# Kernel optimization log

Measured on AMD Instinct MI355X. Metric: run time of the kernel, lower is better.

The kernel has to match this reference:

```python
import jax, jax.numpy as jnp
import numpy as np

B = 256          # batch of molecules
N_ATOM = 1024    # atoms per molecule
N_EDGE = 8192    # directed edges per molecule (avg degree 8)
NEG_SLOPE = 0.01 # torch LeakyReLU default


def setup_inputs() -> dict:
    key = jax.random.key(0)
    ks = jax.random.split(key, 8)
    x = jax.random.normal(ks[0], (B, 3 * N_ATOM), dtype=jnp.float32)
    edge_index = jax.random.randint(ks[1], (2, N_EDGE), 0, N_ATOM, dtype=jnp.int64)
    # GCNConv weights (Glorot-ish small scale) and biases
    W1 = jax.random.normal(ks[2], (3, 64), dtype=jnp.float32) * 0.3
    b1 = jnp.zeros((64,), jnp.float32)
    W2 = jax.random.normal(ks[3], (64, 64), dtype=jnp.float32) * 0.1
    b2 = jnp.zeros((64,), jnp.float32)
    # project MLP: Linear(64,128) + LeakyReLU
    Wp = jax.random.normal(ks[4], (64, 128), dtype=jnp.float32) * 0.1
    bp = jnp.zeros((128,), jnp.float32)
    return {"x": x, "edge_index": edge_index, "W1": W1, "b1": b1,
            "W2": W2, "b2": b2, "Wp": Wp, "bp": bp}


def _leaky_relu(v):
    return jnp.where(v >= 0, v, NEG_SLOPE * v)


def reference(x, edge_index, W1, b1, W2, b2, Wp, bp):
    # x: [B, 3*n_atom] -> node features [B, n_atom, 3]
    bsz, n_feat = x.shape
    n = n_feat // 3
    h = x.reshape(bsz, n, 3)

    src = edge_index[0]  # message sources
    dst = edge_index[1]  # aggregation targets

    # GCN normalization with self-loops: deg[i] = 1 + in-degree(i)
    ones_e = jnp.ones((src.shape[0],), x.dtype)
    deg = jax.ops.segment_sum(ones_e, dst, num_segments=n) + 1.0
    dinv = jax.lax.rsqrt(deg)                # deg^{-1/2}, deg >= 1
    norm_e = dinv[src] * dinv[dst]           # [E]
    norm_self = dinv * dinv                  # self-loop weight per node

    def gcn(h, W, b):
        hw = h @ W                                        # [B, n, d_out]
        msg = hw[:, src, :] * norm_e[None, :, None]       # [B, E, d_out]
        agg = jax.vmap(lambda m: jax.ops.segment_sum(m, dst, num_segments=n))(msg)
        return agg + norm_self[None, :, None] * hw + b

    h = _leaky_relu(gcn(h, W1, b1))
    h = _leaky_relu(gcn(h, W2, b2))

    # global_mean_pool: every graph has exactly n atoms -> mean over atom axis
    g = h.mean(axis=1)                                    # [B, 64]

    # project MLP: Linear + LeakyReLU
    return _leaky_relu(g @ Wp + bp)                       # [B, 128]
```

## Files before the change

### kernel.cpp

```cpp
#include <hip/hip_runtime.h>

#define N_ATOMS 1024
#define N_EDGES 8192
#define EPAD    (N_EDGES + N_ATOMS)
#define NBATCH  256
#define NEG     0.01f

typedef unsigned int u32;
typedef __attribute__((ext_vector_type(2))) float f32x2;
typedef __attribute__((ext_vector_type(4))) float f32x4;
typedef __attribute__((ext_vector_type(8))) _Float16 f16x8;

__device__ __forceinline__ u32 pkrtz(float lo, float hi) {
    u32 r;
    asm("v_cvt_pkrtz_f16_f32 %0, %1, %2" : "=v"(r) : "v"(lo), "v"(hi));
    return r;
}
#define FMIX_LO(a, w, u) \
    asm("v_fma_mix_f32 %0, %1, %2, %0 op_sel_hi:[0,1,0]" : "+v"(a) : "v"(w), "v"(u))
#define FMIX_HI(a, w, u) \
    asm("v_fma_mix_f32 %0, %1, %2, %0 op_sel:[0,1,0] op_sel_hi:[0,1,0]" : "+v"(a) : "v"(w), "v"(u))

#define META_OFF   0
#define COLW_OFF   8192
#define SELFW_OFF  (8192 + 73728)
#define IPERM_OFF  (SELFW_OFF + 4096)
#define W2T_OFF    (IPERM_OFF + 4096)

#define TSTR_B 144
#define SM_TILE_BYTES (N_ATOMS * TSTR_B)
#define SM_CT_OFF SM_TILE_BYTES
#define SM_TOTAL (SM_TILE_BYTES + 16384)

__global__ __launch_bounds__(1024) void build_csr(
    const int* __restrict__ ei,
    int2* __restrict__ colw,
    int2* __restrict__ meta,
    float* __restrict__ selfw_s,
    int*  __restrict__ iperm_g,
    u32*  __restrict__ w2t,
    const float* __restrict__ W2)
{
    __shared__ int   sdeg[N_ATOMS];
    __shared__ int   sstart[N_ATOMS];
    __shared__ int   siperm[N_ATOMS];
    __shared__ float sdinv[N_ATOMS];
    __shared__ int   wtot[16];
    __shared__ int   hist[128];
    const int t = threadIdx.x;
    const int lane = t & 63;
    const int w = t >> 6;
    const int* srcA = ei;
    const int* dstA = ei + N_EDGES;

    sdeg[t] = 0;
    if (t < 128) hist[t] = 0;
    __syncthreads();
    for (int e = t; e < N_EDGES; e += 1024) atomicAdd(&sdeg[dstA[e]], 1);
    __syncthreads();

    const int deg  = sdeg[t];
    const int pdeg = (deg + 1) & ~1;
    int v = pdeg;
    #pragma unroll
    for (int d = 1; d < 64; d <<= 1) {
        int u = __shfl_up(v, d, 64);
        if (lane >= d) v += u;
    }
    if (lane == 63) wtot[w] = v;
    __syncthreads();
    if (t == 0) {
        int run = 0;
        #pragma unroll
        for (int i = 0; i < 16; ++i) { int c = wtot[i]; wtot[i] = run; run += c; }
    }
    __syncthreads();
    const int start = v - pdeg + wtot[w];
    sstart[t] = start;
    const float dv = rsqrtf((float)deg + 1.0f);
    sdinv[t] = dv;
    if (deg & 1) colw[start + deg] = make_int2(0, 0);

    #pragma unroll
    for (int i = 0; i < 2; ++i) {
        const int idx = t + i * 1024;
        const int c = idx >> 5, kk = idx & 31;
        w2t[c * 32 + kk] = pkrtz(W2[(2 * kk) * 64 + c], W2[(2 * kk + 1) * 64 + c]);
    }

    const int dcl = deg < 127 ? deg : 127;
    atomicAdd(&hist[dcl], 1);
    __syncthreads();
    if (t == 0) {
        int run = 0;
        for (int i = 0; i < 128; ++i) { int c = hist[i]; hist[i] = run; run += c; }
    }
    __syncthreads();
    const int pos = atomicAdd(&hist[dcl], 1);
    siperm[t] = pos;
    iperm_g[t] = pos;
    meta[pos] = make_int2(start, pdeg >> 1);
    selfw_s[pos] = dv * dv;
    sdeg[t] = 0;
    __syncthreads();

    for (int e = t; e < N_EDGES; e += 1024) {
        const int d = dstA[e];
        const int s = srcA[e];
        const int slot = atomicAdd(&sdeg[d], 1);
        const float wgt = sdinv[s] * sdinv[d];
        colw[sstart[d] + slot] = make_int2(siperm[s], __float_as_int(wgt));
    }
}

__global__ __launch_bounds__(1024, 4) void gnn_main(
    const float* __restrict__ x,
    const int2* __restrict__ meta,
    const int2* __restrict__ colw,
    const float* __restrict__ selfw_s,
    const int*  __restrict__ iperm_g,
    const float* __restrict__ W1, const float* __restrict__ b1,
    const u32*  __restrict__ w2t, const float* __restrict__ b2,
    const float* __restrict__ Wp, const float* __restrict__ bp,
    float* __restrict__ out)
{
    extern __shared__ char smem[];
    float4* ctile4 = (float4*)(smem + SM_CT_OFF);
    float*  paux   = (float*)ctile4;
    float*  wpool  = paux;
    float*  gvec   = paux + 1024;
    float*  proj   = paux + 1088;

    const int t = threadIdx.x;
    const int b = blockIdx.x;
    const float* xb = x + (size_t)b * (3 * N_ATOMS);

    {
        const int ip = iperm_g[t];
        float4 c;
        c.x = xb[3 * t]; c.y = xb[3 * t + 1]; c.z = xb[3 * t + 2]; c.w = 0.0f;
        ctile4[ip] = c;
    }
    __syncthreads();

    {
        const int2 mt = meta[t];
        const int s0 = mt.x, np1 = mt.y;
        const float sw = selfw_s[t];
        const float4 cs = ctile4[t];
        float A0 = sw * cs.x, A1 = sw * cs.y, A2 = sw * cs.z;
        int4 cur = make_int4(0, 0, 0, 0);
        if (np1 > 0) cur = *(const int4*)(colw + s0);
        for (int jj = 0; jj < np1; ++jj) {
            const int4 nxt = (jj + 1 < np1) ? *(const int4*)(colw + s0 + 2 * (jj + 1)) : cur;
            const float4 c0 = ctile4[cur.x];
            const float4 c1 = ctile4[cur.z];
            const float w0 = __int_as_float(cur.y), w1 = __int_as_float(cur.w);
            A0 += w0 * c0.x + w1 * c1.x;
            A1 += w0 * c0.y + w1 * c1.y;
            A2 += w0 * c0.z + w1 * c1.z;
            cur = nxt;
        }
        u32 pw[32];
        #pragma unroll
        for (int p = 0; p < 32; ++p) {
            f32x2 vv = *(const f32x2*)(b1 + 2 * p);
            vv = __builtin_elementwise_fma((f32x2){A0, A0}, *(const f32x2*)(W1 + 2 * p), vv);
            vv = __builtin_elementwise_fma((f32x2){A1, A1}, *(const f32x2*)(W1 + 64 + 2 * p), vv);
            vv = __builtin_elementwise_fma((f32x2){A2, A2}, *(const f32x2*)(W1 + 128 + 2 * p), vv);
            vv.x = fmaxf(vv.x, NEG * vv.x);
            vv.y = fmaxf(vv.y, NEG * vv.y);
            pw[p] = pkrtz(vv.x, vv.y);
        }
        uint4* trow = (uint4*)(smem + (size_t)t * TSTR_B);
        #pragma unroll
        for (int q = 0; q < 8; ++q)
            trow[q] = make_uint4(pw[4 * q], pw[4 * q + 1], pw[4 * q + 2], pw[4 * q + 3]);
    }

    const int w   = t >> 6;
    const int g   = (t & 63) >> 3;
    const int m   = t & 7;
    const int mo  = m * 16;

    int s0a[8], npa[8];
    float swa[8];
    #pragma unroll
    for (int k = 0; k < 8; ++k) {
        const int slot = k * 128 + w * 8 + g;
        const int2 mk = meta[slot];
        s0a[k] = mk.x;
        npa[k] = mk.y;
        swa[k] = selfw_s[slot];
    }
    __syncthreads();

    u32 pr[8][4];
    #pragma unroll
    for (int k = 0; k < 8; ++k) {
        const int slot = k * 128 + w * 8 + g;
        float acc[8];
        #pragma unroll
        for (int f = 0; f < 8; ++f) acc[f] = 0.0f;
        {
            const float swk = swa[k];
            const uint4 sv = *(const uint4*)(smem + (size_t)slot * TSTR_B + mo);
            FMIX_LO(acc[0], swk, sv.x); FMIX_HI(acc[1], swk, sv.x);
            FMIX_LO(acc[2], swk, sv.y); FMIX_HI(acc[3], swk, sv.y);
            FMIX_LO(acc[4], swk, sv.z); FMIX_HI(acc[5], swk, sv.z);
            FMIX_LO(acc[6], swk, sv.w); FMIX_HI(acc[7], swk, sv.w);
        }
        for (int j = s0a[k]; j < s0a[k] + 2 * npa[k]; j += 2) {
            const int4 cw = *(const int4*)(colw + j);
            const uint4 qA = *(const uint4*)(smem + (size_t)cw.x * TSTR_B + mo);
            const uint4 qB = *(const uint4*)(smem + (size_t)cw.z * TSTR_B + mo);
            const float wA = __int_as_float(cw.y);
            const float wB = __int_as_float(cw.w);
            FMIX_LO(acc[0], wA, qA.x); FMIX_HI(acc[1], wA, qA.x);
            FMIX_LO(acc[2], wA, qA.y); FMIX_HI(acc[3], wA, qA.y);
            FMIX_LO(acc[4], wA, qA.z); FMIX_HI(acc[5], wA, qA.z);
            FMIX_LO(acc[6], wA, qA.w); FMIX_HI(acc[7], wA, qA.w);
            FMIX_LO(acc[0], wB, qB.x); FMIX_HI(acc[1], wB, qB.x);
            FMIX_LO(acc[2], wB, qB.y); FMIX_HI(acc[3], wB, qB.y);
            FMIX_LO(acc[4], wB, qB.z); FMIX_HI(acc[5], wB, qB.z);
            FMIX_LO(acc[6], wB, qB.w); FMIX_HI(acc[7], wB, qB.w);
        }
        pr[k][0] = pkrtz(acc[0], acc[1]);
        pr[k][1] = pkrtz(acc[2], acc[3]);
        pr[k][2] = pkrtz(acc[4], acc[5]);
        pr[k][3] = pkrtz(acc[6], acc[7]);
    }

    const int l15 = t & 15;
    const int lq  = (t & 63) >> 4;
    f16x8 wf[2][4];
    #pragma unroll
    for (int kt = 0; kt < 2; ++kt)
        #pragma unroll
        for (int ct = 0; ct < 4; ++ct)
            wf[kt][ct] = *(const f16x8*)(w2t + (ct * 16 + l15) * 32 + kt * 16 + lq * 4);
    float bias[4];
    #pragma unroll
    for (int ct = 0; ct < 4; ++ct) bias[ct] = b2[ct * 16 + l15];
    float wpv[16];
    {
        const int col = t & 127, pc = (t >> 7) & 3;
        #pragma unroll
        for (int f = 0; f < 16; ++f)
            wpv[f] = Wp[(pc * 16 + f) * 128 + col];
    }

    __syncthreads();

    #pragma unroll
    for (int k = 0; k < 8; ++k) {
        const int slot = k * 128 + w * 8 + g;
        *(uint4*)(smem + (size_t)slot * TSTR_B + mo) =
            make_uint4(pr[k][0], pr[k][1], pr[k][2], pr[k][3]);
    }
    __syncthreads();

    {
        float pool[4] = {0.f, 0.f, 0.f, 0.f};
        #pragma unroll
        for (int rt = 0; rt < 4; ++rt) {
            const int row = w * 64 + rt * 16 + l15;
            const char* ab = smem + (size_t)row * TSTR_B + lq * 16;
            const f16x8 a0 = *(const f16x8*)(ab);
            const f16x8 a1 = *(const f16x8*)(ab + 64);
            #pragma unroll
            for (int ct = 0; ct < 4; ++ct) {
                f32x4 cf = {0.f, 0.f, 0.f, 0.f};
                cf = __builtin_amdgcn_mfma_f32_16x16x32_f16(a0, wf[0][ct], cf, 0, 0, 0);
                cf = __builtin_amdgcn_mfma_f32_16x16x32_f16(a1, wf[1][ct], cf, 0, 0, 0);
                float s = 0.0f;
                #pragma unroll
                for (int r = 0; r < 4; ++r) {
                    const float vv = cf[r] + bias[ct];
                    s += fmaxf(vv, NEG * vv);
                }
                pool[ct] += s;
            }
        }
        #pragma unroll
        for (int ct = 0; ct < 4; ++ct) {
            pool[ct] += __shfl_xor(pool[ct], 16, 64);
            pool[ct] += __shfl_xor(pool[ct], 32, 64);
        }
        if ((t & 63) < 16) {
            #pragma unroll
            for (int ct = 0; ct < 4; ++ct)
                wpool[w * 64 + ct * 16 + l15] = pool[ct];
        }
    }
    __syncthreads();

    if (t < 64) {
        float s = 0.0f;
        #pragma unroll
        for (int ww = 0; ww < 16; ++ww) s += wpool[ww * 64 + t];
        gvec[t] = s * (1.0f / 1024.0f);
    }
    __syncthreads();
    if (t < 512) {
        const int col = t & 127, pc = t >> 7;
        float s = 0.0f;
        #pragma unroll
        for (int f = 0; f < 16; ++f)
            s += gvec[pc * 16 + f] * wpv[f];
        proj[pc * 128 + col] = s;
    }
    __syncthreads();
    if (t < 128) {
        float s = bp[t] + proj[t] + proj[128 + t] + proj[256 + t] + proj[384 + t];
        s = fmaxf(s, NEG * s);
        out[(size_t)b * 128 + t] = s;
    }
}

extern "C" void kernel_launch(void* const* d_in, const int* in_sizes, int n_in,
                              void* d_out, int out_size, void* d_ws, size_t ws_size,
                              hipStream_t stream) {
    const float* x  = (const float*)d_in[0];
    const int*   ei = (const int*)  d_in[1];
    const float* W1 = (const float*)d_in[2];
    const float* b1 = (const float*)d_in[3];
    const float* W2 = (const float*)d_in[4];
    const float* b2 = (const float*)d_in[5];
    const float* Wp = (const float*)d_in[6];
    const float* bp = (const float*)d_in[7];
    float* out = (float*)d_out;

    char* ws = (char*)d_ws;
    int2*  meta   = (int2*) (ws + META_OFF);
    int2*  colw   = (int2*) (ws + COLW_OFF);
    float* selfw  = (float*)(ws + SELFW_OFF);
    int*   iperm  = (int*)  (ws + IPERM_OFF);
    u32*   w2t    = (u32*)  (ws + W2T_OFF);

    build_csr<<<1, 1024, 0, stream>>>(ei, colw, meta, selfw, iperm, w2t, W2);

    (void)hipFuncSetAttribute((const void*)gnn_main,
                              hipFuncAttributeMaxDynamicSharedMemorySize, SM_TOTAL);
    gnn_main<<<NBATCH, 1024, SM_TOTAL, stream>>>(
        x, meta, colw, selfw, iperm, W1, b1, w2t, b2, Wp, bp, out);
}
```

Baseline: 43.13 us.

## Halve block size to 512 threads with two atoms per thread in each stage

```diff
diff --git a/kernel.cpp b/kernel.cpp
--- a/kernel.cpp
+++ b/kernel.cpp
@@ -113,7 +113,7 @@
     }
 }
 
-__global__ __launch_bounds__(1024, 4) void gnn_main(
+__global__ __launch_bounds__(512, 2) void gnn_main(
     const float* __restrict__ x,
     const int2* __restrict__ meta,
     const int2* __restrict__ colw,
@@ -128,111 +128,138 @@
     float4* ctile4 = (float4*)(smem + SM_CT_OFF);
     float*  paux   = (float*)ctile4;
     float*  wpool  = paux;
-    float*  gvec   = paux + 1024;
-    float*  proj   = paux + 1088;
+    float*  gvec   = paux + 512;
+    float*  proj   = paux + 576;
 
     const int t = threadIdx.x;
     const int b = blockIdx.x;
     const float* xb = x + (size_t)b * (3 * N_ATOMS);
 
+    #pragma unroll
+    for (int a = 0; a < 2; ++a) {
+        const int atom = t + a * 512;
+        const int ip = iperm_g[atom];
+        float4 c;
+        c.x = xb[3 * atom]; c.y = xb[3 * atom + 1]; c.z = xb[3 * atom + 2]; c.w = 0.0f;
+        ctile4[ip] = c;
+    }
+    __syncthreads();
+
     {
-        const int ip = iperm_g[t];
-        float4 c;
-        c.x = xb[3 * t]; c.y = xb[3 * t + 1]; c.z = xb[3 * t + 2]; c.w = 0.0f;
-        ctile4[ip] = c;
-    }
-    __syncthreads();
-
-    {
-        const int2 mt = meta[t];
-        const int s0 = mt.x, np1 = mt.y;
-        const float sw = selfw_s[t];
-        const float4 cs = ctile4[t];
-        float A0 = sw * cs.x, A1 = sw * cs.y, A2 = sw * cs.z;
-        int4 cur = make_int4(0, 0, 0, 0);
-        if (np1 > 0) cur = *(const int4*)(colw + s0);
-        for (int jj = 0; jj < np1; ++jj) {
-            const int4 nxt = (jj + 1 < np1) ? *(const int4*)(colw + s0 + 2 * (jj + 1)) : cur;
-            const float4 c0 = ctile4[cur.x];
-            const float4 c1 = ctile4[cur.z];
-            const float w0 = __int_as_float(cur.y), w1 = __int_as_float(cur.w);
-            A0 += w0 * c0.x + w1 * c1.x;
-            A1 += w0 * c0.y + w1 * c1.y;
-            A2 += w0 * c0.z + w1 * c1.z;
-            cur = nxt;
-        }
-        u32 pw[32];
-        #pragma unroll
-        for (int p = 0; p < 32; ++p) {
-            f32x2 vv = *(const f32x2*)(b1 + 2 * p);
-            vv = __builtin_elementwise_fma((f32x2){A0, A0}, *(const f32x2*)(W1 + 2 * p), vv);
-            vv = __builtin_elementwise_fma((f32x2){A1, A1}, *(const f32x2*)(W1 + 64 + 2 * p), vv);
-            vv = __builtin_elementwise_fma((f32x2){A2, A2}, *(const f32x2*)(W1 + 128 + 2 * p), vv);
-            vv.x = fmaxf(vv.x, NEG * vv.x);
-            vv.y = fmaxf(vv.y, NEG * vv.y);
-            pw[p] = pkrtz(vv.x, vv.y);
-        }
-        uint4* trow = (uint4*)(smem + (size_t)t * TSTR_B);
-        #pragma unroll
-        for (int q = 0; q < 8; ++q)
-            trow[q] = make_uint4(pw[4 * q], pw[4 * q + 1], pw[4 * q + 2], pw[4 * q + 3]);
-    }
-
-    const int w   = t >> 6;
-    const int g   = (t & 63) >> 3;
-    const int m   = t & 7;
-    const int mo  = m * 16;
-
-    int s0a[8], npa[8];
-    float swa[8];
-    #pragma unroll
-    for (int k = 0; k < 8; ++k) {
-        const int slot = k * 128 + w * 8 + g;
-        const int2 mk = meta[slot];
-        s0a[k] = mk.x;
-        npa[k] = mk.y;
-        swa[k] = selfw_s[slot];
-    }
-    __syncthreads();
-
-    u32 pr[8][4];
-    #pragma unroll
-    for (int k = 0; k < 8; ++k) {
-        const int slot = k * 128 + w * 8 + g;
-        float acc[8];
-        #pragma unroll
-        for (int f = 0; f < 8; ++f) acc[f] = 0.0f;
-        {
-            const float swk = swa[k];
+        const int2 mA = meta[t];
+        const int2 mB = meta[t + 512];
+        const float swA = selfw_s[t];
+        const float swB = selfw_s[t + 512];
+        const float4 cA = ctile4[t];
+        const float4 cB = ctile4[t + 512];
+        float A0 = swA * cA.x, A1 = swA * cA.y, A2 = swA * cA.z;
+        float B0 = swB * cB.x, B1 = swB * cB.y, B2 = swB * cB.z;
+        const int npA = mA.y, npB = mB.y;
+        const int mx = npA > npB ? npA : npB;
+        for (int jj = 0; jj < mx; ++jj) {
+            if (jj < npA) {
+                const int4 cw = *(const int4*)(colw + mA.x + 2 * jj);
+                const float4 c0 = ctile4[cw.x];
+                const float4 c1 = ctile4[cw.z];
+                const float w0 = __int_as_float(cw.y), w1 = __int_as_float(cw.w);
+                A0 += w0 * c0.x + w1 * c1.x;
+                A1 += w0 * c0.y + w1 * c1.y;
+                A2 += w0 * c0.z + w1 * c1.z;
+            }
+            if (jj < npB) {
+                const int4 cw = *(const int4*)(colw + mB.x + 2 * jj);
+                const float4 c0 = ctile4[cw.x];
+                const float4 c1 = ctile4[cw.z];
+                const float w0 = __int_as_float(cw.y), w1 = __int_as_float(cw.w);
+                B0 += w0 * c0.x + w1 * c1.x;
+                B1 += w0 * c0.y + w1 * c1.y;
+                B2 += w0 * c0.z + w1 * c1.z;
+            }
+        }
+        #pragma unroll
+        for (int a = 0; a < 2; ++a) {
+            const float X0 = a ? B0 : A0, X1 = a ? B1 : A1, X2 = a ? B2 : A2;
+            u32 pw[32];
+            #pragma unroll
+            for (int p = 0; p < 32; ++p) {
+                f32x2 vv = *(const f32x2*)(b1 + 2 * p);
+                vv = __builtin_elementwise_fma((f32x2){X0, X0}, *(const f32x2*)(W1 + 2 * p), vv);
+                vv = __builtin_elementwise_fma((f32x2){X1, X1}, *(const f32x2*)(W1 + 64 + 2 * p), vv);
+                vv = __builtin_elementwise_fma((f32x2){X2, X2}, *(const f32x2*)(W1 + 128 + 2 * p), vv);
+                vv.x = fmaxf(vv.x, NEG * vv.x);
+                vv.y = fmaxf(vv.y, NEG * vv.y);
+                pw[p] = pkrtz(vv.x, vv.y);
+            }
+            uint4* trow = (uint4*)(smem + (size_t)(t + a * 512) * TSTR_B);
+            #pragma unroll
+            for (int q = 0; q < 8; ++q)
+                trow[q] = make_uint4(pw[4 * q], pw[4 * q + 1], pw[4 * q + 2], pw[4 * q + 3]);
+        }
+    }
+    __syncthreads();
+
+    const int G  = t >> 3;
+    const int m  = t & 7;
+    const int mo = m * 16;
+
+    u32 pr[16][4];
+    #pragma unroll
+    for (int p = 0; p < 4; ++p) {
+        int s0a[4], npa[4];
+        float swa[4];
+        #pragma unroll
+        for (int q = 0; q < 4; ++q) {
+            const int slot = (p * 4 + q) * 64 + G;
+            const int2 mk = meta[slot];
+            s0a[q] = mk.x; npa[q] = mk.y;
+            swa[q] = selfw_s[slot];
+        }
+        float acc[32];
+        #pragma unroll
+        for (int f = 0; f < 32; ++f) acc[f] = 0.0f;
+        #pragma unroll
+        for (int q = 0; q < 4; ++q) {
+            const int slot = (p * 4 + q) * 64 + G;
             const uint4 sv = *(const uint4*)(smem + (size_t)slot * TSTR_B + mo);
-            FMIX_LO(acc[0], swk, sv.x); FMIX_HI(acc[1], swk, sv.x);
-            FMIX_LO(acc[2], swk, sv.y); FMIX_HI(acc[3], swk, sv.y);
-            FMIX_LO(acc[4], swk, sv.z); FMIX_HI(acc[5], swk, sv.z);
-            FMIX_LO(acc[6], swk, sv.w); FMIX_HI(acc[7], swk, sv.w);
-        }
-        for (int j = s0a[k]; j < s0a[k] + 2 * npa[k]; j += 2) {
-            const int4 cw = *(const int4*)(colw + j);
-            const uint4 qA = *(const uint4*)(smem + (size_t)cw.x * TSTR_B + mo);
-            const uint4 qB = *(const uint4*)(smem + (size_t)cw.z * TSTR_B + mo);
-            const float wA = __int_as_float(cw.y);
-            const float wB = __int_as_float(cw.w);
-            FMIX_LO(acc[0], wA, qA.x); FMIX_HI(acc[1], wA, qA.x);
-            FMIX_LO(acc[2], wA, qA.y); FMIX_HI(acc[3], wA, qA.y);
-            FMIX_LO(acc[4], wA, qA.z); FMIX_HI(acc[5], wA, qA.z);
-            FMIX_LO(acc[6], wA, qA.w); FMIX_HI(acc[7], wA, qA.w);
-            FMIX_LO(acc[0], wB, qB.x); FMIX_HI(acc[1], wB, qB.x);
-            FMIX_LO(acc[2], wB, qB.y); FMIX_HI(acc[3], wB, qB.y);
-            FMIX_LO(acc[4], wB, qB.z); FMIX_HI(acc[5], wB, qB.z);
-            FMIX_LO(acc[6], wB, qB.w); FMIX_HI(acc[7], wB, qB.w);
-        }
-        pr[k][0] = pkrtz(acc[0], acc[1]);
-        pr[k][1] = pkrtz(acc[2], acc[3]);
-        pr[k][2] = pkrtz(acc[4], acc[5]);
-        pr[k][3] = pkrtz(acc[6], acc[7]);
+            const float swk = swa[q];
+            FMIX_LO(acc[q*8+0], swk, sv.x); FMIX_HI(acc[q*8+1], swk, sv.x);
+            FMIX_LO(acc[q*8+2], swk, sv.y); FMIX_HI(acc[q*8+3], swk, sv.y);
+            FMIX_LO(acc[q*8+4], swk, sv.z); FMIX_HI(acc[q*8+5], swk, sv.z);
+            FMIX_LO(acc[q*8+6], swk, sv.w); FMIX_HI(acc[q*8+7], swk, sv.w);
+        }
+        const int mx = max(max(npa[0], npa[1]), max(npa[2], npa[3]));
+        for (int jj = 0; jj < mx; ++jj) {
+            #pragma unroll
+            for (int q = 0; q < 4; ++q) {
+                if (jj < npa[q]) {
+                    const int4 cw = *(const int4*)(colw + s0a[q] + 2 * jj);
+                    const uint4 qA = *(const uint4*)(smem + (size_t)cw.x * TSTR_B + mo);
+                    const uint4 qB = *(const uint4*)(smem + (size_t)cw.z * TSTR_B + mo);
+                    const float wA = __int_as_float(cw.y);
+                    const float wB = __int_as_float(cw.w);
+                    FMIX_LO(acc[q*8+0], wA, qA.x); FMIX_HI(acc[q*8+1], wA, qA.x);
+                    FMIX_LO(acc[q*8+2], wA, qA.y); FMIX_HI(acc[q*8+3], wA, qA.y);
+                    FMIX_LO(acc[q*8+4], wA, qA.z); FMIX_HI(acc[q*8+5], wA, qA.z);
+                    FMIX_LO(acc[q*8+6], wA, qA.w); FMIX_HI(acc[q*8+7], wA, qA.w);
+                    FMIX_LO(acc[q*8+0], wB, qB.x); FMIX_HI(acc[q*8+1], wB, qB.x);
+                    FMIX_LO(acc[q*8+2], wB, qB.y); FMIX_HI(acc[q*8+3], wB, qB.y);
+                    FMIX_LO(acc[q*8+4], wB, qB.z); FMIX_HI(acc[q*8+5], wB, qB.z);
+                    FMIX_LO(acc[q*8+6], wB, qB.w); FMIX_HI(acc[q*8+7], wB, qB.w);
+                }
+            }
+        }
+        #pragma unroll
+        for (int q = 0; q < 4; ++q) {
+            pr[p*4+q][0] = pkrtz(acc[q*8+0], acc[q*8+1]);
+            pr[p*4+q][1] = pkrtz(acc[q*8+2], acc[q*8+3]);
+            pr[p*4+q][2] = pkrtz(acc[q*8+4], acc[q*8+5]);
+            pr[p*4+q][3] = pkrtz(acc[q*8+6], acc[q*8+7]);
+        }
     }
 
     const int l15 = t & 15;
     const int lq  = (t & 63) >> 4;
+    const int w   = t >> 6;
     f16x8 wf[2][4];
     #pragma unroll
     for (int kt = 0; kt < 2; ++kt)
@@ -242,19 +269,12 @@
     float bias[4];
     #pragma unroll
     for (int ct = 0; ct < 4; ++ct) bias[ct] = b2[ct * 16 + l15];
-    float wpv[16];
-    {
-        const int col = t & 127, pc = (t >> 7) & 3;
-        #pragma unroll
-        for (int f = 0; f < 16; ++f)
-            wpv[f] = Wp[(pc * 16 + f) * 128 + col];
-    }
-
-    __syncthreads();
-
-    #pragma unroll
-    for (int k = 0; k < 8; ++k) {
-        const int slot = k * 128 + w * 8 + g;
+
+    __syncthreads();
+
+    #pragma unroll
+    for (int k = 0; k < 16; ++k) {
+        const int slot = k * 64 + G;
         *(uint4*)(smem + (size_t)slot * TSTR_B + mo) =
             make_uint4(pr[k][0], pr[k][1], pr[k][2], pr[k][3]);
     }
@@ -263,8 +283,8 @@
     {
         float pool[4] = {0.f, 0.f, 0.f, 0.f};
         #pragma unroll
-        for (int rt = 0; rt < 4; ++rt) {
-            const int row = w * 64 + rt * 16 + l15;
+        for (int rt = 0; rt < 8; ++rt) {
+            const int row = w * 128 + rt * 16 + l15;
             const char* ab = smem + (size_t)row * TSTR_B + lq * 16;
             const f16x8 a0 = *(const f16x8*)(ab);
             const f16x8 a1 = *(const f16x8*)(ab + 64);
@@ -298,16 +318,16 @@
     if (t < 64) {
         float s = 0.0f;
         #pragma unroll
-        for (int ww = 0; ww < 16; ++ww) s += wpool[ww * 64 + t];
+        for (int ww = 0; ww < 8; ++ww) s += wpool[ww * 64 + t];
         gvec[t] = s * (1.0f / 1024.0f);
     }
     __syncthreads();
-    if (t < 512) {
+    {
         const int col = t & 127, pc = t >> 7;
         float s = 0.0f;
         #pragma unroll
         for (int f = 0; f < 16; ++f)
-            s += gvec[pc * 16 + f] * wpv[f];
+            s += gvec[pc * 16 + f] * Wp[(pc * 16 + f) * 128 + col];
         proj[pc * 128 + col] = s;
     }
     __syncthreads();
@@ -342,6 +362,6 @@
 
     (void)hipFuncSetAttribute((const void*)gnn_main,
                               hipFuncAttributeMaxDynamicSharedMemorySize, SM_TOTAL);
-    gnn_main<<<NBATCH, 1024, SM_TOTAL, stream>>>(
+    gnn_main<<<NBATCH, 512, SM_TOTAL, stream>>>(
         x, meta, colw, selfw, iperm, W1, b1, w2t, b2, Wp, bp, out);
 }
```

Measured after the change: 47.83 us. 1.11x slower.
